# Kernel optimization log

Measured on AMD Instinct MI355X. Metric: run time of the kernel, lower is better.

The kernel has to match this reference:

```python
import jax, jax.numpy as jnp
import numpy as np

B = 128          # batch of IQ signals
L = 128          # signal length
PL = 16          # patch length
ST = 4           # patch stride
WIN = 4          # local window
NPATCH = (L - PL) // ST + 1   # 29
HID = 256
NCLS = 8
NG = B * NPATCH               # number of patch graphs
N = NG * PL                   # total nodes


def _build_edges():
    src, dst = [], []
    for i in range(PL):
        for j in range(PL):
            if 0 < abs(i - j) <= WIN:
                src.append(i); dst.append(j)
    bs = np.array(src, np.int32)          # [108]
    bd = np.array(dst, np.int32)
    off = (np.arange(NG, dtype=np.int32) * PL)[:, None]
    isrc = (off + bs[None, :]).reshape(-1)
    idst = (off + bd[None, :]).reshape(-1)
    # cross-patch edges: last node of patch p -> first node of patch p+1
    b = np.arange(B, dtype=np.int32)[:, None]
    p = np.arange(NPATCH - 1, dtype=np.int32)[None, :]
    csrc = (b * NPATCH * PL + p * PL + (PL - 1)).reshape(-1)
    cdst = (b * NPATCH * PL + (p + 1) * PL).reshape(-1)
    return np.concatenate([isrc, csrc]), np.concatenate([idst, cdst])


def setup_inputs() -> dict:
    key = jax.random.key(0)
    ks = jax.random.split(key, 10)
    s = 0.05
    esrc, edst = _build_edges()
    return {
        "iq_signal": jax.random.normal(ks[0], (B, 2, L), jnp.float32),
        "edge_src": jnp.asarray(esrc),
        "edge_dst": jnp.asarray(edst),
        # SAGEConv layer 0 (in=2): lin_l (agg, with bias), lin_r (root, no bias)
        "W0_agg": jax.random.normal(ks[1], (HID, 2), jnp.float32) * s,
        "W0_root": jax.random.normal(ks[2], (HID, 2), jnp.float32) * s,
        "b0": jnp.zeros((HID,), jnp.float32),
        # SAGEConv layers 1..3 (256 -> 256), stacked
        "W_agg": jax.random.normal(ks[3], (3, HID, HID), jnp.float32) * s,
        "W_root": jax.random.normal(ks[4], (3, HID, HID), jnp.float32) * s,
        "b_lin": jnp.zeros((3, HID), jnp.float32),
        # per-layer LayerNorms
        "ln_scale": jnp.ones((4, HID), jnp.float32),
        "ln_bias": jnp.zeros((4, HID), jnp.float32),
        # classifier head
        "cls_W1": jax.random.normal(ks[5], (HID, HID), jnp.float32) * s,
        "cls_b1": jnp.zeros((HID,), jnp.float32),
        "cls_ln_scale": jnp.ones((HID,), jnp.float32),
        "cls_ln_bias": jnp.zeros((HID,), jnp.float32),
        "cls_W2": jax.random.normal(ks[6], (NCLS, HID), jnp.float32) * s,
        "cls_b2": jnp.zeros((NCLS,), jnp.float32),
    }


def _ln(x, g, b):
    m = x.mean(-1, keepdims=True)
    v = ((x - m) ** 2).mean(-1, keepdims=True)
    return (x - m) * jax.lax.rsqrt(v + 1e-5) * g + b


def reference(iq_signal, edge_src, edge_dst, W0_agg, W0_root, b0,
              W_agg, W_root, b_lin, ln_scale, ln_bias,
              cls_W1, cls_b1, cls_ln_scale, cls_ln_bias, cls_W2, cls_b2):
    # patch extraction: [B,2,L] -> [B,NPATCH,PL,2] -> node features [N,2]
    idx = jnp.arange(NPATCH)[:, None] * ST + jnp.arange(PL)[None, :]   # [29,16]
    x = jnp.transpose(iq_signal[:, :, idx], (0, 2, 3, 1)).reshape(-1, 2)

    # in-degree for mean aggregation (0 -> safe divide by 1)
    ones = jnp.ones((edge_dst.shape[0],), x.dtype)
    deg = jax.ops.segment_sum(ones, edge_dst, num_segments=N)
    inv_deg = 1.0 / jnp.maximum(deg, 1.0)

    def sage(h, Wa, Wr, b):
        # mean-aggregate neighbor messages, then lin_l(agg) + lin_r(h) + bias
        agg = jax.ops.segment_sum(h[edge_src], edge_dst, num_segments=N)
        agg = agg * inv_deg[:, None]
        return agg @ Wa.T + h @ Wr.T + b

    # layer 0 (2 -> 256): no residual (shape change)
    h = jax.nn.relu(_ln(sage(x, W0_agg, W0_root, b0), ln_scale[0], ln_bias[0]))
    # layers 1..3 with residual
    for l in range(3):
        hn = jax.nn.relu(_ln(sage(h, W_agg[l], W_root[l], b_lin[l]),
                             ln_scale[l + 1], ln_bias[l + 1]))
        h = h + hn

    node_emb = h                                  # [N, 256]
    # global_mean_pool per patch graph (16 consecutive nodes each)
    gf = node_emb.reshape(NG, PL, HID).mean(axis=1)   # [NG, 256]
    z = jax.nn.relu(_ln(gf @ cls_W1.T + cls_b1, cls_ln_scale, cls_ln_bias))
    logits = z @ cls_W2.T + cls_b2                # [NG, 8]
    return logits, gf, node_emb
```

## Files before the change

### kernel.cpp

```cpp
#include <hip/hip_runtime.h>
#include <hip/hip_bf16.h>

typedef __hip_bfloat16 bf16;
typedef unsigned short u16;
typedef unsigned int uint32;
typedef __attribute__((ext_vector_type(8))) short bf16x8;
typedef __attribute__((ext_vector_type(4))) float f32x4;

#define BATCH   128
#define LSIG    128
#define PL      16
#define ST      4
#define WIN     4
#define NPATCH  29
#define NG      (BATCH * NPATCH)
#define NNODE   (NG * PL)
#define HID     256
#define NCLS    8

#define IQ_OFF    0
#define W0A_OFF   32768
#define W0R_OFF   33280
#define B0_OFF    33792
#define BLIN_OFF  34048
#define LNS_OFF   34816
#define LNB_OFF   35840
#define W1T_OFF   36864
#define CB1_OFF   102400
#define CLNS_OFF  102656
#define CLNB_OFF  102912
#define CW2_OFF   103168
#define CB2_OFF   105216
#define CVT_TOTAL 105224

#define P_BYTE_OFF   4096
#define WB_BYTE_OFF  425984
#define A_BYTE_OFF   1216512
#define B_BYTE_OFF   1959936
#define GF_EOFF      (NG * NCLS)
#define EMB_EOFF     (NG * NCLS + NG * HID)

#define MFMA_BF16 __builtin_amdgcn_mfma_f32_16x16x32_bf16

__device__ __forceinline__ float b2f(bf16 x) { return __bfloat162float(x); }
__device__ __forceinline__ float lof(uint32 u) { return __uint_as_float(u << 16); }
__device__ __forceinline__ float hif(uint32 u) { return __uint_as_float(u & 0xFFFF0000u); }
__device__ __forceinline__ uint32 packbf(float a, float b) {
  bf16 r0 = __float2bfloat16(a), r1 = __float2bfloat16(b);
  return ((uint32)(*(const u16*)&r1) << 16) | (uint32)(*(const u16*)&r0);
}
__device__ __forceinline__ float ldmix(const void* p, size_t i, int fl) {
  return fl ? ((const float*)p)[i] : __bfloat162float(((const bf16*)p)[i]);
}

__global__ __launch_bounds__(256) void detect_kernel(const u16* __restrict__ iq, int* flag) {
  __shared__ int sbig, snz;
  int t = threadIdx.x;
  if (t == 0) { sbig = 0; snz = 0; }
  __syncthreads();
  int big = 0, nz = 0;
  for (int e = t; e < 16384; e += 256) {
    u16 u = iq[2 * e];
    int ex = (u >> 7) & 0xFF;
    if (ex >= 0xC0) big++;
    if (u != 0) nz++;
  }
  atomicAdd(&sbig, big); atomicAdd(&snz, nz);
  __syncthreads();
  if (t == 0) *flag = (sbig > 4 || snz < 100) ? 1 : 0;
}

__global__ __launch_bounds__(256) void convert_params(
    const int* __restrict__ flag,
    const void* iq, const void* w0a, const void* w0r, const void* b0,
    const void* blin, const void* lns, const void* lnb,
    const void* cw1, const void* cb1, const void* clns, const void* clnb,
    const void* cw2, const void* cb2,
    float* __restrict__ P) {
  int idx = blockIdx.x * 256 + threadIdx.x;
  if (idx >= CVT_TOTAL) return;
  int fl = *flag;
  float v;
  if (idx < W0A_OFF)        v = ldmix(iq,  idx, fl);
  else if (idx < W0R_OFF)   v = ldmix(w0a, idx - W0A_OFF, fl);
  else if (idx < B0_OFF)    v = ldmix(w0r, idx - W0R_OFF, fl);
  else if (idx < BLIN_OFF)  v = ldmix(b0,  idx - B0_OFF, fl);
  else if (idx < LNS_OFF)   v = ldmix(blin, idx - BLIN_OFF, fl);
  else if (idx < LNB_OFF)   v = ldmix(lns, idx - LNS_OFF, fl);
  else if (idx < W1T_OFF)   v = ldmix(lnb, idx - LNB_OFF, fl);
  else if (idx < CB1_OFF) { int t2 = idx - W1T_OFF;
    v = ldmix(cw1, (t2 & 255) * 256 + (t2 >> 8), fl); }
  else if (idx < CLNS_OFF)  v = ldmix(cb1, idx - CB1_OFF, fl);
  else if (idx < CLNB_OFF)  v = ldmix(clns, idx - CLNS_OFF, fl);
  else if (idx < CW2_OFF)   v = ldmix(clnb, idx - CLNB_OFF, fl);
  else if (idx < CB2_OFF)   v = ldmix(cw2, idx - CW2_OFF, fl);
  else                      v = ldmix(cb2, idx - CB2_OFF, fl);
  P[idx] = v;
}

__global__ __launch_bounds__(256) void convert_wb(
    const int* __restrict__ flag, const void* wag, const void* wro, bf16* __restrict__ WB) {
  int idx = blockIdx.x * 256 + threadIdx.x;
  int fl = *flag;
  int l = idx >> 17, m = (idx >> 16) & 1, r = idx & 65535;
  const void* src = m ? wro : wag;
  WB[idx] = __float2bfloat16(ldmix(src, l * 65536 + r, fl));
}

__global__ __launch_bounds__(256) void layer0_kernel(
    const float* __restrict__ P, bf16* __restrict__ hout) {
  int g = blockIdx.x, f = threadIdx.x;
  int b = g / NPATCH, p = g % NPATCH;
  __shared__ float x_s[PL][2];
  __shared__ float xp_s[2];
  __shared__ float agg_s[PL][2];
  __shared__ float o_s[PL][HID];
  __shared__ float mv_s[PL][2];
  if (f < 32) { int j = f & 15, c = f >> 4;
    x_s[j][c] = P[IQ_OFF + (b * 2 + c) * LSIG + p * ST + j]; }
  if (f < 2) xp_s[f] = (p > 0) ? P[IQ_OFF + (b * 2 + f) * LSIG + (p - 1) * ST + PL - 1] : 0.f;
  __syncthreads();
  if (f < 32) { int j = f & 15, c = f >> 4;
    float s = 0.f;
    int lo = j - WIN < 0 ? 0 : j - WIN, hi = j + WIN > 15 ? 15 : j + WIN;
    for (int i = lo; i <= hi; ++i) if (i != j) s += x_s[i][c];
    int deg = (j < WIN ? j : WIN) + ((15 - j) < WIN ? (15 - j) : WIN);
    if (j == 0 && p > 0) { s += xp_s[c]; deg += 1; }
    agg_s[j][c] = s / (float)deg;
  }
  __syncthreads();
  float wa0 = P[W0A_OFF + f * 2], wa1 = P[W0A_OFF + f * 2 + 1];
  float wr0 = P[W0R_OFF + f * 2], wr1 = P[W0R_OFF + f * 2 + 1];
  float bb = P[B0_OFF + f];
#pragma unroll
  for (int j = 0; j < PL; ++j)
    o_s[j][f] = agg_s[j][0] * wa0 + agg_s[j][1] * wa1 + x_s[j][0] * wr0 + x_s[j][1] * wr1 + bb;
  __syncthreads();
  { int j = f >> 4, q = f & 15;
    float s = 0.f, s2 = 0.f;
#pragma unroll
    for (int i = 0; i < 16; ++i) { float v = o_s[j][q + 16 * i]; s += v; s2 += v * v; }
#pragma unroll
    for (int m = 8; m >= 1; m >>= 1) { s += __shfl_xor(s, m); s2 += __shfl_xor(s2, m); }
    if (q == 0) { float mean = s * (1.f / HID);
      float var = s2 * (1.f / HID) - mean * mean;
      mv_s[j][0] = mean; mv_s[j][1] = rsqrtf(var + 1e-5f); }
  }
  __syncthreads();
  float gl = P[LNS_OFF + f], bl = P[LNB_OFF + f];
#pragma unroll
  for (int j = 0; j < PL; ++j) {
    float v = (o_s[j][f] - mv_s[j][0]) * mv_s[j][1] * gl + bl;
    v = v > 0.f ? v : 0.f;
    hout[(size_t)(g * PL + j) * HID + f] = __float2bfloat16(v);
  }
}

template<int LAST>
__global__ __launch_bounds__(256, 2) void sage_mfma(
    const bf16* __restrict__ hin,
    const bf16* __restrict__ Wa, const bf16* __restrict__ Wr,
    const float* __restrict__ bias,
    const float* __restrict__ lng, const float* __restrict__ lnb,
    bf16* __restrict__ hout,
    void* __restrict__ dout, const int* __restrict__ flag) {
  int t = threadIdx.x;
  int w = t >> 6, l = t & 63, lr = l & 15, lg = l >> 4;
  int g0 = blockIdx.x * 4;
  size_t nbase = (size_t)g0 * PL;
  __shared__ uint32 h32[64 * 128];
  __shared__ uint32 a32[64 * 128];
  float* mvp = (float*)h32;
  const uint32* hinw = (const uint32*)hin;

  const uint32* hg = hinw + nbase * 128;
#pragma unroll
  for (int it = 0; it < 8; ++it) {
    int u = it * 256 + t;
    int row = u >> 5, sl = u & 31;
    int sw = sl ^ (row & 7);
    *(uint4*)&h32[row * 128 + sw * 4] = *(const uint4*)(hg + u * 4);
  }
  __syncthreads();

  {
    int c2 = t & 127, Ph = t >> 7;
#pragma unroll
    for (int pi = 0; pi < 2; ++pi) {
      int pp = Ph + pi * 2;
      int pr = pp * 16;
      int hp = ((g0 + pp) % NPATCH) != 0;
      float vlo[16], vhi[16];
#pragma unroll
      for (int j = 0; j < 16; ++j) {
        uint32 u = h32[(pr + j) * 128 + (((c2 >> 2) ^ (j & 7)) << 2) + (c2 & 3)];
        vlo[j] = lof(u); vhi[j] = hif(u);
      }
      float blo = 0.f, bhi = 0.f;
      if (hp) {
        uint32 u;
        if (pp == 0) u = hinw[(nbase - 1) * 128 + c2];
        else { int br = pr - 1;
          u = h32[br * 128 + (((c2 >> 2) ^ (br & 7)) << 2) + (c2 & 3)]; }
        blo = lof(u); bhi = hif(u);
      }
#pragma unroll
      for (int j = 0; j < 16; ++j) {
        const int a = (j - WIN < 0) ? 0 : j - WIN;
        const int b = (j + WIN > 15) ? 15 : j + WIN;
        float slo = 0.f, shi = 0.f;
#pragma unroll
        for (int i = 0; i < 16; ++i)
          if (i >= a && i <= b && i != j) { slo += vlo[i]; shi += vhi[i]; }
        float deg = (float)((j < WIN ? j : WIN) + (15 - j < WIN ? 15 - j : WIN));
        if (j == 0 && hp) { slo += blo; shi += bhi; deg += 1.f; }
        float inv = 1.f / deg;
        a32[(pr + j) * 128 + (((c2 >> 2) ^ (j & 7)) << 2) + (c2 & 3)] = packbf(slo * inv, shi * inv);
      }
    }
  }
  __syncthreads();

  f32x4 acc[4][4];
#pragma unroll
  for (int m = 0; m < 4; ++m)
#pragma unroll
    for (int n = 0; n < 4; ++n) acc[m][n] = (f32x4){0.f, 0.f, 0.f, 0.f};
  int colbase = w * 64;
  const bf16* waB = Wa + (colbase + lr) * HID + lg * 8;
  const bf16* wrB = Wr + (colbase + lr) * HID + lg * 8;
  bf16x8 wafr[2][4], wrfr[2][4];
#pragma unroll
  for (int nt = 0; nt < 4; ++nt) {
    wafr[0][nt] = *(const bf16x8*)(waB + nt * 16 * HID);
    wrfr[0][nt] = *(const bf16x8*)(wrB + nt * 16 * HID);
  }
#pragma unroll
  for (int ks = 0; ks < 8; ++ks) {
    const int cur = ks & 1, nxt = cur ^ 1;
    if (ks < 7) {
#pragma unroll
      for (int nt = 0; nt < 4; ++nt) {
        wafr[nxt][nt] = *(const bf16x8*)(waB + nt * 16 * HID + (ks + 1) * 32);
        wrfr[nxt][nt] = *(const bf16x8*)(wrB + nt * 16 * HID + (ks + 1) * 32);
      }
    }
#pragma unroll
    for (int m = 0; m < 4; ++m) {
      int idx = (m * 16 + lr) * 128 + (((ks * 4 + lg) ^ (lr & 7)) << 2);
      bf16x8 af = *(const bf16x8*)&a32[idx];
      bf16x8 hf = *(const bf16x8*)&h32[idx];
#pragma unroll
      for (int nt = 0; nt < 4; ++nt) {
        acc[m][nt] = MFMA_BF16(af, wafr[cur][nt], acc[m][nt], 0, 0, 0);
        acc[m][nt] = MFMA_BF16(hf, wrfr[cur][nt], acc[m][nt], 0, 0, 0);
      }
    }
  }
#pragma unroll
  for (int nt = 0; nt < 4; ++nt) {
    float bv = bias[colbase + nt * 16 + lr];
#pragma unroll
    for (int m = 0; m < 4; ++m) {
      acc[m][nt][0] += bv; acc[m][nt][1] += bv; acc[m][nt][2] += bv; acc[m][nt][3] += bv;
    }
  }
  __syncthreads();

#pragma unroll
  for (int m = 0; m < 4; ++m)
#pragma unroll
    for (int nt = 0; nt < 4; ++nt) {
      int col = colbase + nt * 16 + lr;
#pragma unroll
      for (int r = 0; r < 4; ++r) {
        int row = m * 16 + lg * 4 + r;
        int i16 = row * 256 + (((col >> 3) ^ (row & 7)) << 3) + (col & 7);
        bf16 x = __float2bfloat16(acc[m][nt][r]);
        ((u16*)a32)[i16] = *(const u16*)&x;
      }
    }
  __syncthreads();

  {
    int row = t >> 2, q = t & 3;
    float s = 0.f, s2 = 0.f;
#pragma unroll
    for (int i = 0; i < 32; ++i) {
      int d = q * 32 + i;
      uint32 u = a32[row * 128 + (((d >> 2) ^ (row & 7)) << 2) + (d & 3)];
      float a = lof(u), b = hif(u);
      s += a + b; s2 += a * a + b * b;
    }
    s += __shfl_xor(s, 1); s2 += __shfl_xor(s2, 1);
    s += __shfl_xor(s, 2); s2 += __shfl_xor(s2, 2);
    if (q == 0) { float mean = s * (1.f / HID);
      mvp[row * 2] = mean;
      mvp[row * 2 + 1] = rsqrtf(s2 * (1.f / HID) - mean * mean + 1e-5f); }
  }
  __syncthreads();

  {
    int c2 = t & 127, prt = t >> 7;
    float gl0 = lng[c2 * 2], gl1 = lng[c2 * 2 + 1];
    float bl0 = lnb[c2 * 2], bl1 = lnb[c2 * 2 + 1];
    uint32* outw = nullptr;
    if constexpr (!LAST) outw = (uint32*)hout + nbase * 128;
    const uint32* inw = hinw + nbase * 128;
    int fl = 0;
    if constexpr (LAST) fl = *flag;
#pragma unroll
    for (int pi = 0; pi < 2; ++pi) {
      float sga = 0.f, sgb = 0.f;
#pragma unroll
      for (int i = 0; i < 16; ++i) {
        int row = prt * 32 + pi * 16 + i;
        uint32 u = a32[row * 128 + (((c2 >> 2) ^ (row & 7)) << 2) + (c2 & 3)];
        float mean = mvp[row * 2], rstd = mvp[row * 2 + 1];
        float a = (lof(u) - mean) * rstd * gl0 + bl0; a = a > 0.f ? a : 0.f;
        float b_ = (hif(u) - mean) * rstd * gl1 + bl1; b_ = b_ > 0.f ? b_ : 0.f;
        uint32 hu = inw[row * 128 + c2];
        a += lof(hu); b_ += hif(hu);
        if constexpr (!LAST) {
          outw[row * 128 + c2] = packbf(a, b_);
        } else {
          sga += a; sgb += b_;
          if (fl) {
            size_t ei = (size_t)EMB_EOFF + (nbase + row) * 256 + (size_t)c2 * 2;
            ((float*)dout)[ei] = a; ((float*)dout)[ei + 1] = b_;
          } else {
            ((uint32*)dout)[(EMB_EOFF >> 1) + (nbase + row) * 128 + c2] = packbf(a, b_);
          }
        }
      }
      if constexpr (LAST) {
        float ga = sga * (1.f / PL), gb = sgb * (1.f / PL);
        int gidx = g0 + prt * 2 + pi;
        if (fl) {
          size_t gi = (size_t)GF_EOFF + (size_t)gidx * 256 + (size_t)c2 * 2;
          ((float*)dout)[gi] = ga; ((float*)dout)[gi + 1] = gb;
        } else {
          ((uint32*)dout)[(GF_EOFF >> 1) + gidx * 128 + c2] = packbf(ga, gb);
        }
      }
    }
  }
}

__global__ __launch_bounds__(256) void head_kernel(
    const void* __restrict__ gin, const float* __restrict__ P,
    void* __restrict__ dout, const int* __restrict__ flag) {
  int g = blockIdx.x, f = threadIdx.x;
  int fl = *flag;
  __shared__ float gf_s[HID];
  __shared__ float z_s[HID];
  __shared__ float ps[4], ps2[4];
  __shared__ float mr[2];
  gf_s[f] = fl ? ((const float*)gin)[(size_t)GF_EOFF + (size_t)g * HID + f]
               : b2f(((const bf16*)gin)[(size_t)GF_EOFF + (size_t)g * HID + f]);
  __syncthreads();
  float acc = P[CB1_OFF + f];
  for (int k = 0; k < HID; k += 4) {
    const float4 gv = *(const float4*)(&gf_s[k]);
    acc = fmaf(gv.x, P[W1T_OFF + (k + 0) * HID + f], acc);
    acc = fmaf(gv.y, P[W1T_OFF + (k + 1) * HID + f], acc);
    acc = fmaf(gv.z, P[W1T_OFF + (k + 2) * HID + f], acc);
    acc = fmaf(gv.w, P[W1T_OFF + (k + 3) * HID + f], acc);
  }
  float s1 = acc, s2 = acc * acc;
#pragma unroll
  for (int m = 32; m >= 1; m >>= 1) { s1 += __shfl_xor(s1, m); s2 += __shfl_xor(s2, m); }
  int wid = f >> 6, lane = f & 63;
  if (lane == 0) { ps[wid] = s1; ps2[wid] = s2; }
  __syncthreads();
  if (f == 0) {
    float S = ps[0] + ps[1] + ps[2] + ps[3];
    float S2 = ps2[0] + ps2[1] + ps2[2] + ps2[3];
    float mean = S * (1.f / HID);
    mr[0] = mean; mr[1] = rsqrtf(S2 * (1.f / HID) - mean * mean + 1e-5f);
  }
  __syncthreads();
  float z = (acc - mr[0]) * mr[1] * P[CLNS_OFF + f] + P[CLNB_OFF + f];
  z = z > 0.f ? z : 0.f;
  z_s[f] = z;
  __syncthreads();
  if (f < NCLS) {
    float a = P[CB2_OFF + f];
    for (int k = 0; k < HID; ++k) a = fmaf(z_s[k], P[CW2_OFF + f * HID + k], a);
    size_t ei = (size_t)g * NCLS + f;
    if (fl) ((float*)dout)[ei] = a; else ((bf16*)dout)[ei] = __float2bfloat16(a);
  }
}

extern "C" void kernel_launch(void* const* d_in, const int* in_sizes, int n_in,
                              void* d_out, int out_size, void* d_ws, size_t ws_size,
                              hipStream_t stream) {
  char* ws = (char*)d_ws;
  int*   flag = (int*)ws;
  float* P    = (float*)(ws + P_BYTE_OFF);
  bf16*  WB   = (bf16*)(ws + WB_BYTE_OFF);
  bf16*  A    = (bf16*)(ws + A_BYTE_OFF);
  bf16*  B    = (bf16*)((char*)d_out + B_BYTE_OFF);

  detect_kernel<<<1, 256, 0, stream>>>((const u16*)d_in[0], flag);
  convert_params<<<(CVT_TOTAL + 255) / 256, 256, 0, stream>>>(
      flag, d_in[0], d_in[3], d_in[4], d_in[5], d_in[8],
      d_in[9], d_in[10], d_in[11], d_in[12], d_in[13], d_in[14], d_in[15], d_in[16], P);
  convert_wb<<<1536, 256, 0, stream>>>(flag, d_in[6], d_in[7], WB);

  layer0_kernel<<<NG, 256, 0, stream>>>(P, A);
  sage_mfma<0><<<NG / 4, 256, 0, stream>>>(A, WB, WB + 65536,
      P + BLIN_OFF, P + LNS_OFF + HID, P + LNB_OFF + HID, B, nullptr, flag);
  sage_mfma<0><<<NG / 4, 256, 0, stream>>>(B, WB + 131072, WB + 131072 + 65536,
      P + BLIN_OFF + HID, P + LNS_OFF + 2 * HID, P + LNB_OFF + 2 * HID, A, nullptr, flag);
  sage_mfma<1><<<NG / 4, 256, 0, stream>>>(A, WB + 262144, WB + 262144 + 65536,
      P + BLIN_OFF + 2 * HID, P + LNS_OFF + 3 * HID, P + LNB_OFF + 3 * HID, nullptr, d_out, flag);
  head_kernel<<<NG, 256, 0, stream>>>(d_out, P, d_out, flag);
}
```

Before: 240.7 us.

## Reuse one LDS buffer: root GEMM first, aggregate in place, fused LN stats

The SAGE layer kernel now uses a single 32KB LDS tile instead of two. It runs the root GEMM (h @ Wr) first, then overwrites the same buffer with the mean-aggregated neighbours and runs the aggregation GEMM into the same accumulators. LayerNorm statistics are computed straight from the MFMA accumulators with wave shuffles and a small cross-wave partial-sum array, which removes a separate LDS reduction pass. Weight fragments are reloaded per k-step instead of double-buffered. This halves LDS use so more blocks can be resident per CU, at the cost of an extra barrier and less latency hiding on the weight loads.

```diff
diff --git a/kernel.cpp b/kernel.cpp
--- a/kernel.cpp
+++ b/kernel.cpp
@@ -168,56 +168,25 @@
   int w = t >> 6, l = t & 63, lr = l & 15, lg = l >> 4;
   int g0 = blockIdx.x * 4;
   size_t nbase = (size_t)g0 * PL;
-  __shared__ uint32 h32[64 * 128];
-  __shared__ uint32 a32[64 * 128];
-  float* mvp = (float*)h32;
+  __shared__ uint32 hb[64 * 128];
+  __shared__ float part_s[64][4][2];
+  __shared__ float mv_s[64][2];
   const uint32* hinw = (const uint32*)hin;
+
+  int colbase = w * 64;
+  const bf16* waB = Wa + (colbase + lr) * HID + lg * 8;
+  const bf16* wrB = Wr + (colbase + lr) * HID + lg * 8;
+
+  bf16x8 w0f[8];
+#pragma unroll
+  for (int ks = 0; ks < 8; ++ks) w0f[ks] = *(const bf16x8*)(wrB + ks * 32);
 
   const uint32* hg = hinw + nbase * 128;
 #pragma unroll
   for (int it = 0; it < 8; ++it) {
     int u = it * 256 + t;
     int row = u >> 5, sl = u & 31;
-    int sw = sl ^ (row & 7);
-    *(uint4*)&h32[row * 128 + sw * 4] = *(const uint4*)(hg + u * 4);
-  }
-  __syncthreads();
-
-  {
-    int c2 = t & 127, Ph = t >> 7;
-#pragma unroll
-    for (int pi = 0; pi < 2; ++pi) {
-      int pp = Ph + pi * 2;
-      int pr = pp * 16;
-      int hp = ((g0 + pp) % NPATCH) != 0;
-      float vlo[16], vhi[16];
-#pragma unroll
-      for (int j = 0; j < 16; ++j) {
-        uint32 u = h32[(pr + j) * 128 + (((c2 >> 2) ^ (j & 7)) << 2) + (c2 & 3)];
-        vlo[j] = lof(u); vhi[j] = hif(u);
-      }
-      float blo = 0.f, bhi = 0.f;
-      if (hp) {
-        uint32 u;
-        if (pp == 0) u = hinw[(nbase - 1) * 128 + c2];
-        else { int br = pr - 1;
-          u = h32[br * 128 + (((c2 >> 2) ^ (br & 7)) << 2) + (c2 & 3)]; }
-        blo = lof(u); bhi = hif(u);
-      }
-#pragma unroll
-      for (int j = 0; j < 16; ++j) {
-        const int a = (j - WIN < 0) ? 0 : j - WIN;
-        const int b = (j + WIN > 15) ? 15 : j + WIN;
-        float slo = 0.f, shi = 0.f;
-#pragma unroll
-        for (int i = 0; i < 16; ++i)
-          if (i >= a && i <= b && i != j) { slo += vlo[i]; shi += vhi[i]; }
-        float deg = (float)((j < WIN ? j : WIN) + (15 - j < WIN ? 15 - j : WIN));
-        if (j == 0 && hp) { slo += blo; shi += bhi; deg += 1.f; }
-        float inv = 1.f / deg;
-        a32[(pr + j) * 128 + (((c2 >> 2) ^ (j & 7)) << 2) + (c2 & 3)] = packbf(slo * inv, shi * inv);
-      }
-    }
+    *(uint4*)&hb[row * 128 + ((sl ^ (row & 7)) << 2)] = *(const uint4*)(hg + u * 4);
   }
   __syncthreads();
 
@@ -226,37 +195,84 @@
   for (int m = 0; m < 4; ++m)
 #pragma unroll
     for (int n = 0; n < 4; ++n) acc[m][n] = (f32x4){0.f, 0.f, 0.f, 0.f};
-  int colbase = w * 64;
-  const bf16* waB = Wa + (colbase + lr) * HID + lg * 8;
-  const bf16* wrB = Wr + (colbase + lr) * HID + lg * 8;
-  bf16x8 wafr[2][4], wrfr[2][4];
-#pragma unroll
-  for (int nt = 0; nt < 4; ++nt) {
-    wafr[0][nt] = *(const bf16x8*)(waB + nt * 16 * HID);
-    wrfr[0][nt] = *(const bf16x8*)(wrB + nt * 16 * HID);
-  }
 #pragma unroll
   for (int ks = 0; ks < 8; ++ks) {
-    const int cur = ks & 1, nxt = cur ^ 1;
-    if (ks < 7) {
-#pragma unroll
-      for (int nt = 0; nt < 4; ++nt) {
-        wafr[nxt][nt] = *(const bf16x8*)(waB + nt * 16 * HID + (ks + 1) * 32);
-        wrfr[nxt][nt] = *(const bf16x8*)(wrB + nt * 16 * HID + (ks + 1) * 32);
-      }
-    }
+    bf16x8 w1 = *(const bf16x8*)(wrB + 1 * 16 * HID + ks * 32);
+    bf16x8 w2 = *(const bf16x8*)(wrB + 2 * 16 * HID + ks * 32);
+    bf16x8 w3 = *(const bf16x8*)(wrB + 3 * 16 * HID + ks * 32);
 #pragma unroll
     for (int m = 0; m < 4; ++m) {
-      int idx = (m * 16 + lr) * 128 + (((ks * 4 + lg) ^ (lr & 7)) << 2);
-      bf16x8 af = *(const bf16x8*)&a32[idx];
-      bf16x8 hf = *(const bf16x8*)&h32[idx];
-#pragma unroll
-      for (int nt = 0; nt < 4; ++nt) {
-        acc[m][nt] = MFMA_BF16(af, wafr[cur][nt], acc[m][nt], 0, 0, 0);
-        acc[m][nt] = MFMA_BF16(hf, wrfr[cur][nt], acc[m][nt], 0, 0, 0);
-      }
-    }
-  }
+      bf16x8 hf = *(const bf16x8*)&hb[(m * 16 + lr) * 128 + (((ks * 4 + lg) ^ (lr & 7)) << 2)];
+      acc[m][0] = MFMA_BF16(hf, w0f[ks], acc[m][0], 0, 0, 0);
+      acc[m][1] = MFMA_BF16(hf, w1, acc[m][1], 0, 0, 0);
+      acc[m][2] = MFMA_BF16(hf, w2, acc[m][2], 0, 0, 0);
+      acc[m][3] = MFMA_BF16(hf, w3, acc[m][3], 0, 0, 0);
+    }
+  }
+
+  bf16x8 a0f[8];
+#pragma unroll
+  for (int ks = 0; ks < 8; ++ks) a0f[ks] = *(const bf16x8*)(waB + ks * 32);
+
+  int c2 = t & 127, Ph = t >> 7;
+  uint32 bnd[2];
+#pragma unroll
+  for (int pi = 0; pi < 2; ++pi) {
+    int pp = Ph + pi * 2;
+    int hp = ((g0 + pp) % NPATCH) != 0;
+    uint32 u = 0;
+    if (hp) {
+      if (pp == 0) u = hinw[(nbase - 1) * 128 + c2];
+      else { int br = pp * 16 - 1;
+        u = hb[br * 128 + (((c2 >> 2) ^ (br & 7)) << 2) + (c2 & 3)]; }
+    }
+    bnd[pi] = u;
+  }
+  __syncthreads();
+
+#pragma unroll
+  for (int pi = 0; pi < 2; ++pi) {
+    int pp = Ph + pi * 2;
+    int pr = pp * 16;
+    int hp = ((g0 + pp) % NPATCH) != 0;
+    float vlo[16], vhi[16];
+#pragma unroll
+    for (int j = 0; j < 16; ++j) {
+      uint32 u = hb[(pr + j) * 128 + (((c2 >> 2) ^ (j & 7)) << 2) + (c2 & 3)];
+      vlo[j] = lof(u); vhi[j] = hif(u);
+    }
+    float blo = lof(bnd[pi]), bhi = hif(bnd[pi]);
+#pragma unroll
+    for (int j = 0; j < 16; ++j) {
+      const int a = (j - WIN < 0) ? 0 : j - WIN;
+      const int b = (j + WIN > 15) ? 15 : j + WIN;
+      float slo = 0.f, shi = 0.f;
+#pragma unroll
+      for (int i = 0; i < 16; ++i)
+        if (i >= a && i <= b && i != j) { slo += vlo[i]; shi += vhi[i]; }
+      float deg = (float)((j < WIN ? j : WIN) + (15 - j < WIN ? 15 - j : WIN));
+      if (j == 0 && hp) { slo += blo; shi += bhi; deg += 1.f; }
+      float inv = 1.f / deg;
+      hb[(pr + j) * 128 + (((c2 >> 2) ^ (j & 7)) << 2) + (c2 & 3)] = packbf(slo * inv, shi * inv);
+    }
+  }
+  __syncthreads();
+
+#pragma unroll
+  for (int ks = 0; ks < 8; ++ks) {
+    bf16x8 w1 = *(const bf16x8*)(waB + 1 * 16 * HID + ks * 32);
+    bf16x8 w2 = *(const bf16x8*)(waB + 2 * 16 * HID + ks * 32);
+    bf16x8 w3 = *(const bf16x8*)(waB + 3 * 16 * HID + ks * 32);
+#pragma unroll
+    for (int m = 0; m < 4; ++m) {
+      bf16x8 af = *(const bf16x8*)&hb[(m * 16 + lr) * 128 + (((ks * 4 + lg) ^ (lr & 7)) << 2)];
+      acc[m][0] = MFMA_BF16(af, a0f[ks], acc[m][0], 0, 0, 0);
+      acc[m][1] = MFMA_BF16(af, w1, acc[m][1], 0, 0, 0);
+      acc[m][2] = MFMA_BF16(af, w2, acc[m][2], 0, 0, 0);
+      acc[m][3] = MFMA_BF16(af, w3, acc[m][3], 0, 0, 0);
+    }
+  }
+
 #pragma unroll
   for (int nt = 0; nt < 4; ++nt) {
     float bv = bias[colbase + nt * 16 + lr];
@@ -265,8 +281,28 @@
       acc[m][nt][0] += bv; acc[m][nt][1] += bv; acc[m][nt][2] += bv; acc[m][nt][3] += bv;
     }
   }
-  __syncthreads();
-
+#pragma unroll
+  for (int m = 0; m < 4; ++m)
+#pragma unroll
+    for (int r = 0; r < 4; ++r) {
+      float s = acc[m][0][r] + acc[m][1][r] + acc[m][2][r] + acc[m][3][r];
+      float s2 = acc[m][0][r] * acc[m][0][r] + acc[m][1][r] * acc[m][1][r]
+               + acc[m][2][r] * acc[m][2][r] + acc[m][3][r] * acc[m][3][r];
+      s += __shfl_xor(s, 1); s2 += __shfl_xor(s2, 1);
+      s += __shfl_xor(s, 2); s2 += __shfl_xor(s2, 2);
+      s += __shfl_xor(s, 4); s2 += __shfl_xor(s2, 4);
+      s += __shfl_xor(s, 8); s2 += __shfl_xor(s2, 8);
+      if (lr == 0) { int row = m * 16 + lg * 4 + r; part_s[row][w][0] = s; part_s[row][w][1] = s2; }
+    }
+  __syncthreads();
+
+  if (t < 64) {
+    float S = part_s[t][0][0] + part_s[t][1][0] + part_s[t][2][0] + part_s[t][3][0];
+    float S2 = part_s[t][0][1] + part_s[t][1][1] + part_s[t][2][1] + part_s[t][3][1];
+    float mean = S * (1.f / HID);
+    mv_s[t][0] = mean;
+    mv_s[t][1] = rsqrtf(S2 * (1.f / HID) - mean * mean + 1e-5f);
+  }
 #pragma unroll
   for (int m = 0; m < 4; ++m)
 #pragma unroll
@@ -277,31 +313,13 @@
         int row = m * 16 + lg * 4 + r;
         int i16 = row * 256 + (((col >> 3) ^ (row & 7)) << 3) + (col & 7);
         bf16 x = __float2bfloat16(acc[m][nt][r]);
-        ((u16*)a32)[i16] = *(const u16*)&x;
+        ((u16*)hb)[i16] = *(const u16*)&x;
       }
     }
   __syncthreads();
 
   {
-    int row = t >> 2, q = t & 3;
-    float s = 0.f, s2 = 0.f;
-#pragma unroll
-    for (int i = 0; i < 32; ++i) {
-      int d = q * 32 + i;
-      uint32 u = a32[row * 128 + (((d >> 2) ^ (row & 7)) << 2) + (d & 3)];
-      float a = lof(u), b = hif(u);
-      s += a + b; s2 += a * a + b * b;
-    }
-    s += __shfl_xor(s, 1); s2 += __shfl_xor(s2, 1);
-    s += __shfl_xor(s, 2); s2 += __shfl_xor(s2, 2);
-    if (q == 0) { float mean = s * (1.f / HID);
-      mvp[row * 2] = mean;
-      mvp[row * 2 + 1] = rsqrtf(s2 * (1.f / HID) - mean * mean + 1e-5f); }
-  }
-  __syncthreads();
-
-  {
-    int c2 = t & 127, prt = t >> 7;
+    int prt = t >> 7;
     float gl0 = lng[c2 * 2], gl1 = lng[c2 * 2 + 1];
     float bl0 = lnb[c2 * 2], bl1 = lnb[c2 * 2 + 1];
     uint32* outw = nullptr;
@@ -315,8 +333,8 @@
 #pragma unroll
       for (int i = 0; i < 16; ++i) {
         int row = prt * 32 + pi * 16 + i;
-        uint32 u = a32[row * 128 + (((c2 >> 2) ^ (row & 7)) << 2) + (c2 & 3)];
-        float mean = mvp[row * 2], rstd = mvp[row * 2 + 1];
+        uint32 u = hb[row * 128 + (((c2 >> 2) ^ (row & 7)) << 2) + (c2 & 3)];
+        float mean = mv_s[row][0], rstd = mv_s[row][1];
         float a = (lof(u) - mean) * rstd * gl0 + bl0; a = a > 0.f ? a : 0.f;
         float b_ = (hif(u) - mean) * rstd * gl1 + bl1; b_ = b_ > 0.f ? b_ : 0.f;
         uint32 hu = inw[row * 128 + c2];
```

Result: slower. 246.6 us (+2.5%).
